# Optimization experiments

Measured on AMD Instinct MI355X. Metric: run time of the kernel, lower is better.

## Reference

```python
import jax, jax.numpy as jnp
import numpy as np
from jax import lax

T_STEPS = 16
TAU = 2.0
ALPHA = 4.0  # sigmoid surrogate sharpness
BN_EPS = 1e-5


def conv1d(x, w, b, stride, pad):
    # x: [N,C,L], w: [O,I,K]
    y = lax.conv_general_dilated(x, w, (stride,), [(pad, pad)],
                                 dimension_numbers=('NCH', 'OIH', 'NCH'))
    return y + b[None, :, None]


def maxpool1d(x):  # kernel 3, stride 2, pad 1 (pad value -inf via init)
    return lax.reduce_window(x, -jnp.inf, lax.max, (1, 1, 3), (1, 1, 2),
                             [(0, 0), (0, 0), (1, 1)])


def spike(x):  # heaviside forward (surrogate only matters for bwd)
    return (x >= 0).astype(x.dtype)


def lif(x_seq):
    # multi-step LIF: v += (x - v)/tau (v_reset=0), spike at v>=1, hard reset, detach_reset
    def step(v, x):
        v = v + (x - v) / TAU
        s = spike(v - 1.0)
        v = v * (1.0 - lax.stop_gradient(s))
        return v, s
    _, s_seq = lax.scan(step, jnp.zeros_like(x_seq[0]), x_seq)
    return s_seq


def seq_apply(f, xs):
    # apply stateless layer over [T,B,...] by folding T into batch
    T, B = xs.shape[0], xs.shape[1]
    y = f(xs.reshape((T * B,) + xs.shape[2:]))
    return y.reshape((T, B) + y.shape[1:])


def setup_inputs() -> dict:
    key = jax.random.key(0)
    ks = jax.random.split(key, 12)
    B, L = 256, 4097
    inp = {
        'x': jax.random.normal(ks[0], (B, L), jnp.float32),
        'conv0_w': jax.random.normal(ks[1], (16, 1, 7), jnp.float32) * 0.2,
        'conv0_b': jax.random.normal(ks[2], (16,), jnp.float32) * 0.1,
        'bn_g': jnp.ones((16,), jnp.float32),
        'bn_b': jnp.zeros((16,), jnp.float32),
        'bn_m': jax.random.normal(ks[3], (16,), jnp.float32) * 0.1,
        'bn_v': jnp.ones((16,), jnp.float32),
        'conv1_w': jax.random.normal(ks[4], (32, 16, 5), jnp.float32) * 0.1,
        'conv1_b': jax.random.normal(ks[5], (32,), jnp.float32) * 0.1,
        'conv2_w': jax.random.normal(ks[6], (64, 32, 3), jnp.float32) * 0.1,
        'conv2_b': jax.random.normal(ks[7], (64,), jnp.float32) * 0.1,
        'fc1_w': jax.random.normal(ks[8], (32, 64), jnp.float32) * 0.12,
        'fc1_b': jax.random.normal(ks[9], (32,), jnp.float32) * 0.1,
        'fc2_w': jax.random.normal(ks[10], (5, 32), jnp.float32) * 0.17,
        'fc2_b': jax.random.normal(ks[11], (5,), jnp.float32) * 0.1,
    }
    return inp


def reference(x, conv0_w, conv0_b, bn_g, bn_b, bn_m, bn_v,
              conv1_w, conv1_b, conv2_w, conv2_b,
              fc1_w, fc1_b, fc2_w, fc2_b):
    # ---- static encoder ----
    h = x[:, None, :]                                  # [B,1,4097]
    h = conv1d(h, conv0_w, conv0_b, 2, 3)              # [B,16,2049]
    h = (h - bn_m[None, :, None]) * lax.rsqrt(bn_v + BN_EPS)[None, :, None] \
        * bn_g[None, :, None] + bn_b[None, :, None]
    h = jax.nn.relu(h)
    h = maxpool1d(h)                                   # [B,16,1025]
    # ---- repeat over T timesteps ----
    hs = jnp.broadcast_to(h[None], (T_STEPS,) + h.shape)  # [T,B,16,1025]
    # ---- spiking trunk ----
    hs = seq_apply(lambda a: conv1d(a, conv1_w, conv1_b, 2, 2), hs)  # [T,B,32,513]
    hs = lif(hs)
    hs = seq_apply(maxpool1d, hs)                      # [T,B,32,257]
    hs = seq_apply(lambda a: conv1d(a, conv2_w, conv2_b, 2, 1), hs)  # [T,B,64,129]
    hs = lif(hs)
    # dropout: identity (inference); adaptive avg pool to 1 + flatten
    hs = hs.mean(axis=-1)                              # [T,B,64]
    # ---- classifier ----
    hs = jnp.einsum('tbd,od->tbo', hs, fc1_w) + fc1_b  # [T,B,32]
    hs = lif(hs)
    hs = jnp.einsum('tbd,od->tbo', hs, fc2_w) + fc2_b  # [T,B,5]
    return hs.mean(axis=0)                             # [B,5]
```

## Files before the change

### kernel.cpp

```cpp
#include <hip/hip_runtime.h>
#include <math.h>


#define NB 256
#define LX 4097
#define LQ 2049
#define LP 1025
#define LJ1 513
#define LP1 257
#define LJ2 129

#define M1S 520
#define S2R 132
#define JT 64
#define NJT 9
#define HSW 132
#define XSN 544

typedef float f32x4 __attribute__((ext_vector_type(4)));

__global__ __launch_bounds__(256) void kS_setup(const float* __restrict__ w1,
                                                const float* __restrict__ w2,
                                                float* __restrict__ w1t,
                                                float* __restrict__ w2t2) {
  int tid = threadIdx.x;
  for (int i = tid; i < 2560; i += 256) {
    int c = i & 31, r = i >> 5;
    w1t[i] = w1[c * 80 + r];
  }
  for (int idx = tid; idx < 64 * 32 * 3; idx += 256) {
    int k = idx % 3; int r = idx / 3; int cc = r % 32; int oc = r / 32;
    w2t2[((size_t)cc * 64 + oc) * 4 + k] = w2[idx];
  }
}

__global__ __launch_bounds__(256) void kF_front(const float* __restrict__ x,
                                                const float* __restrict__ w0,
                                                const float* __restrict__ b0,
                                                const float* __restrict__ bng,
                                                const float* __restrict__ bnb,
                                                const float* __restrict__ bnm,
                                                const float* __restrict__ bnv,
                                                const float* __restrict__ w1t_g,
                                                const float* __restrict__ b1,
                                                unsigned short* __restrict__ m1) {
  __shared__ __align__(16) float xs[XSN];
  __shared__ __align__(16) float hs[16 * HSW];
  __shared__ float w0s[112];
  __shared__ float cpar[64];
  __shared__ float rs_l[16];
  int bid = blockIdx.x;
  int b = bid / NJT, jt = bid % NJT;
  int J0 = jt * JT;
  int Pstart = 2 * J0 - 2;
  int tid = threadIdx.x;

  if (tid < 16) rs_l[tid] = (float)(1.0 / sqrt((double)bnv[tid] + 1e-5));
  {
    const float* xb = x + (size_t)b * LX;
    int xoff = 4 * Pstart - 5;
    for (int i = tid; i < XSN; i += 256) {
      int gi = xoff + i;
      xs[i] = (gi >= 0 && gi < LX) ? xb[gi] : 0.f;
    }
    if (tid < 112) w0s[tid] = w0[tid];
    if (tid >= 128 && tid < 192) {
      int i = tid - 128;
      int c = i >> 2, e = i & 3;
      float v = (e == 0) ? bnm[c] : (e == 1) ? bng[c] : (e == 2) ? bnb[c] : b0[c];
      cpar[i] = v;
    }
  }
  __syncthreads();

  {
    int c2 = tid >> 4, g2 = tid & 15;
    float m = cpar[4 * c2], g = cpar[4 * c2 + 1], bb = cpar[4 * c2 + 2],
          bc = cpar[4 * c2 + 3];
    float rs = rs_l[c2];
    float wv[7];
#pragma unroll
    for (int k = 0; k < 7; ++k) wv[k] = w0s[c2 * 7 + k];
    int dp0 = g2 * 9;
    const f32x4* xv = (const f32x4*)xs;
    f32x4 q0 = xv[dp0], q1 = xv[dp0 + 1], q2 = xv[dp0 + 2];
#pragma unroll
    for (int i = 0; i < 9; ++i) {
      int dp = dp0 + i;
      if (dp >= 132) break;
      int p = Pstart + dp;
      float hm = 0.f;
      if (p >= 0 && p < LP) {
        float win[12] = {q0.x, q0.y, q0.z, q0.w, q1.x, q1.y, q1.z, q1.w,
                         q2.x, q2.y, q2.z, q2.w};
        float best = -INFINITY;
#pragma unroll
        for (int dq = -1; dq <= 1; ++dq) {
          int q = 2 * p + dq;
          if (q < 0 || q >= LQ) continue;
          float s = 0.f;
          int base = 2 * dq + 2;
#pragma unroll
          for (int k = 0; k < 7; ++k) s = fmaf(win[base + k], wv[k], s);
          float y = s + bc;
          y = (y - m) * rs * g + bb;
          y = fmaxf(y, 0.f);
          best = fmaxf(best, y);
        }
        hm = best;
      }
      hs[c2 * HSW + dp] = hm;
      q0 = q1; q1 = q2; q2 = xv[dp + 3];
    }
  }
  __syncthreads();

  {
    int c = tid & 31, jg = tid >> 5;
    int jbase = J0 + jg * 8;
    if (jbase <= 512) {
      float acc[8];
#pragma unroll
      for (int i = 0; i < 8; ++i) acc[i] = 0.f;

#pragma unroll 1
      for (int ic = 0; ic < 16; ++ic) {
        float win[20];
        const f32x4* row = (const f32x4*)(hs + ic * HSW + 16 * jg);
#pragma unroll
        for (int i = 0; i < 5; ++i) {
          f32x4 v = row[i];
          win[4 * i] = v.x; win[4 * i + 1] = v.y;
          win[4 * i + 2] = v.z; win[4 * i + 3] = v.w;
        }
        float wv[5];
#pragma unroll
        for (int k = 0; k < 5; ++k) wv[k] = w1t_g[(ic * 5 + k) * 32 + c];
#pragma unroll
        for (int j = 0; j < 8; ++j) {
#pragma unroll
          for (int k = 0; k < 5; ++k) acc[j] = fmaf(win[2 * j + k], wv[k], acc[j]);
        }
      }

      float bc = b1[c];
      unsigned mskv[8];
#pragma unroll
      for (int j = 0; j < 8; ++j) {
        float xin = acc[j] + bc;
        float v = 0.f; unsigned mm = 0;
#pragma unroll
        for (int t = 0; t < 16; ++t) {
          v = v + (xin - v) * 0.5f;
          if (v >= 1.f) { mm |= (1u << t); v = 0.f; }
        }
        mskv[j] = mm;
      }
      size_t rowo = ((size_t)b * 32 + c) * M1S + jbase;
      if (jbase + 7 < LJ1) {
        uint4 u0;
        u0.x = mskv[0] | (mskv[1] << 16);
        u0.y = mskv[2] | (mskv[3] << 16);
        u0.z = mskv[4] | (mskv[5] << 16);
        u0.w = mskv[6] | (mskv[7] << 16);
        *(uint4*)(m1 + rowo) = u0;
      } else {
        for (int j = 0; j < 8; ++j)
          if (jbase + j < LJ1) m1[rowo + j] = (unsigned short)mskv[j];
      }
    }
  }
}

__global__ __launch_bounds__(256) void kD_conv2_lif(const unsigned short* __restrict__ m1,
                                                    const float* __restrict__ w2t2,
                                                    const float* __restrict__ b2,
                                                    unsigned short* __restrict__ s2) {
  __shared__ __align__(16) float F[288 * 20];
  __shared__ unsigned mval[288];
  int bid = blockIdx.x;
  int b = bid / 33, jt = bid % 33;
  int j0 = jt * 4;
  int tid = threadIdx.x;
  int w = tid >> 6;
  int lane = tid & 63;

  const unsigned short* m1b = m1 + (size_t)b * 32 * M1S;

  for (int it = tid; it < 288; it += 256) {
    int c = it / 9, idx = it - c * 9;
    int p = 2 * j0 - 1 + idx;
    unsigned m = 0;
    if (p >= 0 && p < LP1) {
      const unsigned short* mr = m1b + (size_t)c * M1S;
      int q0 = 2 * p - 1;
      if (q0 >= 0) m |= mr[q0];
      m |= mr[q0 + 1];
      if (q0 + 2 <= 512) m |= mr[q0 + 2];
    }
    mval[it] = m;
    f32x4* Fr = (f32x4*)(F + it * 20);
    f32x4 f0, f1, f2, f3;
    f0.x = (float)(m & 1u);         f0.y = (float)((m >> 1) & 1u);
    f0.z = (float)((m >> 2) & 1u);  f0.w = (float)((m >> 3) & 1u);
    f1.x = (float)((m >> 4) & 1u);  f1.y = (float)((m >> 5) & 1u);
    f1.z = (float)((m >> 6) & 1u);  f1.w = (float)((m >> 7) & 1u);
    f2.x = (float)((m >> 8) & 1u);  f2.y = (float)((m >> 9) & 1u);
    f2.z = (float)((m >> 10) & 1u); f2.w = (float)((m >> 11) & 1u);
    f3.x = (float)((m >> 12) & 1u); f3.y = (float)((m >> 13) & 1u);
    f3.z = (float)((m >> 14) & 1u); f3.w = (float)((m >> 15) & 1u);
    Fr[0] = f0; Fr[1] = f1; Fr[2] = f2; Fr[3] = f3;
  }
  __syncthreads();

  unsigned bits;
  {
    bool nz = false;
    if (lane < 32) {
      int base9 = lane * 9 + 2 * w;
      nz = (mval[base9] | mval[base9 + 1] | mval[base9 + 2]) != 0u;
    }
    bits = (unsigned)__ballot(nz);
  }

  float acc[16];
#pragma unroll
  for (int t = 0; t < 16; ++t) acc[t] = 0.f;

  const f32x4* wbase = (const f32x4*)w2t2 + lane;
  while (bits) {
    int c = __builtin_ctz(bits);
    bits &= bits - 1;
    int base9 = c * 9 + 2 * w;
    unsigned mv0 = mval[base9];
    unsigned mv1 = mval[base9 + 1];
    unsigned mv2 = mval[base9 + 2];
    f32x4 wq = wbase[c * 64];
    const float* Fb = F + base9 * 20;
    if (mv0) {
      const f32x4* Fp = (const f32x4*)Fb;
      f32x4 fv[4];
      fv[0] = Fp[0]; fv[1] = Fp[1]; fv[2] = Fp[2]; fv[3] = Fp[3];
#pragma unroll
      for (int t = 0; t < 16; ++t) acc[t] = fmaf(wq.x, fv[t >> 2][t & 3], acc[t]);
    }
    if (mv1) {
      const f32x4* Fp = (const f32x4*)(Fb + 20);
      f32x4 fv[4];
      fv[0] = Fp[0]; fv[1] = Fp[1]; fv[2] = Fp[2]; fv[3] = Fp[3];
#pragma unroll
      for (int t = 0; t < 16; ++t) acc[t] = fmaf(wq.y, fv[t >> 2][t & 3], acc[t]);
    }
    if (mv2) {
      const f32x4* Fp = (const f32x4*)(Fb + 40);
      f32x4 fv[4];
      fv[0] = Fp[0]; fv[1] = Fp[1]; fv[2] = Fp[2]; fv[3] = Fp[3];
#pragma unroll
      for (int t = 0; t < 16; ++t) acc[t] = fmaf(wq.z, fv[t >> 2][t & 3], acc[t]);
    }
  }

  int j = j0 + w;
  if (j < LJ2) {
    float bc = b2[lane];
    float v = 0.f; unsigned mm = 0;
#pragma unroll
    for (int t = 0; t < 16; ++t) {
      float xin = acc[t] + bc;
      v = v + (xin - v) * 0.5f;
      if (v >= 1.f) { mm |= (1u << t); v = 0.f; }
    }
    s2[((size_t)b * S2R + j) * 64 + lane] = (unsigned short)mm;
  }
}

__global__ __launch_bounds__(256) void kE_head(const unsigned short* __restrict__ s2,
                                               const float* __restrict__ fc1w,
                                               const float* __restrict__ fc1b,
                                               const float* __restrict__ fc2w,
                                               const float* __restrict__ fc2b,
                                               float* __restrict__ out) {
  __shared__ unsigned cntL[4][16][64];
  __shared__ float meanL[16][64];
  __shared__ unsigned s3m[32];
  int b = blockIdx.x;
  int tid = threadIdx.x;
  int w = tid >> 6, lane = tid & 63;

  int j0 = (w == 0) ? 0 : 33 + 32 * (w - 1);
  int jc = (w == 0) ? 33 : 32;
  const unsigned short* base = s2 + (size_t)b * S2R * 64 + lane;
  unsigned cnt[16];
#pragma unroll
  for (int t = 0; t < 16; ++t) cnt[t] = 0;
  for (int u = 0; u < jc; ++u) {
    unsigned m = base[(size_t)(j0 + u) * 64];
#pragma unroll
    for (int t = 0; t < 16; ++t) cnt[t] += (m >> t) & 1u;
  }
#pragma unroll
  for (int t = 0; t < 16; ++t) cntL[w][t][lane] = cnt[t];
  __syncthreads();

#pragma unroll
  for (int i = 0; i < 4; ++i) {
    int idx = tid + 256 * i;
    int t = idx >> 6, oc = idx & 63;
    unsigned s = cntL[0][t][oc] + cntL[1][t][oc] + cntL[2][t][oc] + cntL[3][t][oc];
    meanL[t][oc] = (float)s / 129.f;
  }
  __syncthreads();

  if (tid < 32) {
    int o = tid;
    const float* wrow = fc1w + o * 64;
    float bb = fc1b[o];
    float v = 0.f;
    unsigned msk = 0;
    for (int t = 0; t < 16; ++t) {
      float s = 0.f;
      for (int d = 0; d < 64; ++d) s = fmaf(meanL[t][d], wrow[d], s);
      float xin = s + bb;
      v = v + (xin - v) * 0.5f;
      if (v >= 1.f) { msk |= (1u << t); v = 0.f; }
    }
    s3m[o] = msk;
  }
  __syncthreads();

  if (tid < 5) {
    int q = tid;
    const float* wrow = fc2w + q * 32;
    float bb = fc2b[q];
    float accs = 0.f;
    for (int t = 0; t < 16; ++t) {
      float s = 0.f;
      for (int o = 0; o < 32; ++o) s += (((s3m[o] >> t) & 1u) ? wrow[o] : 0.f);
      accs += (s + bb);
    }
    out[b * 5 + q] = accs / 16.f;
  }
}

extern "C" void kernel_launch(void* const* d_in, const int* in_sizes, int n_in,
                              void* d_out, int out_size, void* d_ws, size_t ws_size,
                              hipStream_t stream) {
  const float* x   = (const float*)d_in[0];
  const float* w0  = (const float*)d_in[1];
  const float* b0  = (const float*)d_in[2];
  const float* bng = (const float*)d_in[3];
  const float* bnb = (const float*)d_in[4];
  const float* bnm = (const float*)d_in[5];
  const float* bnv = (const float*)d_in[6];
  const float* w1  = (const float*)d_in[7];
  const float* b1  = (const float*)d_in[8];
  const float* w2  = (const float*)d_in[9];
  const float* b2  = (const float*)d_in[10];
  const float* f1w = (const float*)d_in[11];
  const float* f1b = (const float*)d_in[12];
  const float* f2w = (const float*)d_in[13];
  const float* f2b = (const float*)d_in[14];
  float* out = (float*)d_out;

  char* ws = (char*)d_ws;
  size_t sz_m1 = (size_t)NB * 32 * M1S * 2;
  size_t sz_s2 = (size_t)NB * S2R * 64 * 2;
  size_t off_s2 = sz_m1;
  size_t off_w2 = off_s2 + sz_s2;
  size_t off_w1 = off_w2 + 32768;
  if (ws_size < off_w1 + 10240) return;

  unsigned short* m1 = (unsigned short*)ws;
  unsigned short* s2 = (unsigned short*)(ws + off_s2);
  float* w2t2 = (float*)(ws + off_w2);
  float* w1t  = (float*)(ws + off_w1);

  kS_setup<<<1, 256, 0, stream>>>(w1, w2, w1t, w2t2);
  kF_front<<<NB * NJT, 256, 0, stream>>>(x, w0, b0, bng, bnb, bnm, bnv, w1t, b1, m1);
  kD_conv2_lif<<<NB * 33, 256, 0, stream>>>(m1, w2t2, b2, s2);
  kE_head<<<NB, 256, 0, stream>>>(s2, f1w, f1b, f2w, f2b, out);
}
```

Measured before the change: 108.8 us.

## Fold weight setup kernel into front kernel and stage conv1 weights in LDS

Drops the single-block setup kernel. Each front-kernel block now loads and transposes conv1 weights into shared memory itself, and the first 16 blocks write the transposed conv2 weights for the next kernel. This removes one launch and its serialization, and turns the global weight reads in the conv1 inner loop into shared-memory reads. The cost is extra per-block weight loading and about 10KB more LDS per block, which may reduce occupancy. The conv2 kernel also replaces per-iteration LDS mask reads with three ballots.

```diff
diff --git a/kernel.cpp b/kernel.cpp
--- a/kernel.cpp
+++ b/kernel.cpp
@@ -19,21 +19,6 @@
 
 typedef float f32x4 __attribute__((ext_vector_type(4)));
 
-__global__ __launch_bounds__(256) void kS_setup(const float* __restrict__ w1,
-                                                const float* __restrict__ w2,
-                                                float* __restrict__ w1t,
-                                                float* __restrict__ w2t2) {
-  int tid = threadIdx.x;
-  for (int i = tid; i < 2560; i += 256) {
-    int c = i & 31, r = i >> 5;
-    w1t[i] = w1[c * 80 + r];
-  }
-  for (int idx = tid; idx < 64 * 32 * 3; idx += 256) {
-    int k = idx % 3; int r = idx / 3; int cc = r % 32; int oc = r / 32;
-    w2t2[((size_t)cc * 64 + oc) * 4 + k] = w2[idx];
-  }
-}
-
 __global__ __launch_bounds__(256) void kF_front(const float* __restrict__ x,
                                                 const float* __restrict__ w0,
                                                 const float* __restrict__ b0,
@@ -41,11 +26,14 @@
                                                 const float* __restrict__ bnb,
                                                 const float* __restrict__ bnm,
                                                 const float* __restrict__ bnv,
-                                                const float* __restrict__ w1t_g,
+                                                const float* __restrict__ w1,
                                                 const float* __restrict__ b1,
-                                                unsigned short* __restrict__ m1) {
+                                                unsigned short* __restrict__ m1,
+                                                const float* __restrict__ w2,
+                                                float* __restrict__ w2t2) {
   __shared__ __align__(16) float xs[XSN];
   __shared__ __align__(16) float hs[16 * HSW];
+  __shared__ __align__(16) float wl[2560];
   __shared__ float w0s[112];
   __shared__ float cpar[64];
   __shared__ float rs_l[16];
@@ -62,6 +50,9 @@
     for (int i = tid; i < XSN; i += 256) {
       int gi = xoff + i;
       xs[i] = (gi >= 0 && gi < LX) ? xb[gi] : 0.f;
+    }
+    for (int i = tid; i < 2560; i += 256) {
+      wl[i] = w1[(i & 31) * 80 + (i >> 5)];
     }
     if (tid < 112) w0s[tid] = w0[tid];
     if (tid >= 128 && tid < 192) {
@@ -135,7 +126,7 @@
         }
         float wv[5];
 #pragma unroll
-        for (int k = 0; k < 5; ++k) wv[k] = w1t_g[(ic * 5 + k) * 32 + c];
+        for (int k = 0; k < 5; ++k) wv[k] = wl[(ic * 5 + k) * 32 + c];
 #pragma unroll
         for (int j = 0; j < 8; ++j) {
 #pragma unroll
@@ -170,6 +161,13 @@
       }
     }
   }
+
+  if (bid < 16) {
+    for (int idx = bid * 256 + tid; idx < 64 * 32 * 3; idx += 4096) {
+      int k = idx % 3; int r = idx / 3; int cc = r % 32; int oc = r / 32;
+      w2t2[((size_t)cc * 64 + oc) * 4 + k] = w2[idx];
+    }
+  }
 }
 
 __global__ __launch_bounds__(256) void kD_conv2_lif(const unsigned short* __restrict__ m1,
@@ -213,15 +211,17 @@
   }
   __syncthreads();
 
-  unsigned bits;
-  {
-    bool nz = false;
-    if (lane < 32) {
-      int base9 = lane * 9 + 2 * w;
-      nz = (mval[base9] | mval[base9 + 1] | mval[base9 + 2]) != 0u;
-    }
-    bits = (unsigned)__ballot(nz);
-  }
+  bool nz0 = false, nz1 = false, nz2 = false;
+  if (lane < 32) {
+    int mb = lane * 9 + 2 * w;
+    nz0 = mval[mb] != 0u;
+    nz1 = mval[mb + 1] != 0u;
+    nz2 = mval[mb + 2] != 0u;
+  }
+  unsigned bz0 = (unsigned)__ballot(nz0);
+  unsigned bz1 = (unsigned)__ballot(nz1);
+  unsigned bz2 = (unsigned)__ballot(nz2);
+  unsigned bits = bz0 | bz1 | bz2;
 
   float acc[16];
 #pragma unroll
@@ -232,26 +232,23 @@
     int c = __builtin_ctz(bits);
     bits &= bits - 1;
     int base9 = c * 9 + 2 * w;
-    unsigned mv0 = mval[base9];
-    unsigned mv1 = mval[base9 + 1];
-    unsigned mv2 = mval[base9 + 2];
     f32x4 wq = wbase[c * 64];
     const float* Fb = F + base9 * 20;
-    if (mv0) {
+    if ((bz0 >> c) & 1u) {
       const f32x4* Fp = (const f32x4*)Fb;
       f32x4 fv[4];
       fv[0] = Fp[0]; fv[1] = Fp[1]; fv[2] = Fp[2]; fv[3] = Fp[3];
 #pragma unroll
       for (int t = 0; t < 16; ++t) acc[t] = fmaf(wq.x, fv[t >> 2][t & 3], acc[t]);
     }
-    if (mv1) {
+    if ((bz1 >> c) & 1u) {
       const f32x4* Fp = (const f32x4*)(Fb + 20);
       f32x4 fv[4];
       fv[0] = Fp[0]; fv[1] = Fp[1]; fv[2] = Fp[2]; fv[3] = Fp[3];
 #pragma unroll
       for (int t = 0; t < 16; ++t) acc[t] = fmaf(wq.y, fv[t >> 2][t & 3], acc[t]);
     }
-    if (mv2) {
+    if ((bz2 >> c) & 1u) {
       const f32x4* Fp = (const f32x4*)(Fb + 40);
       f32x4 fv[4];
       fv[0] = Fp[0]; fv[1] = Fp[1]; fv[2] = Fp[2]; fv[3] = Fp[3];
@@ -367,16 +364,13 @@
   size_t sz_s2 = (size_t)NB * S2R * 64 * 2;
   size_t off_s2 = sz_m1;
   size_t off_w2 = off_s2 + sz_s2;
-  size_t off_w1 = off_w2 + 32768;
-  if (ws_size < off_w1 + 10240) return;
+  if (ws_size < off_w2 + 32768) return;
 
   unsigned short* m1 = (unsigned short*)ws;
   unsigned short* s2 = (unsigned short*)(ws + off_s2);
   float* w2t2 = (float*)(ws + off_w2);
-  float* w1t  = (float*)(ws + off_w1);
-
-  kS_setup<<<1, 256, 0, stream>>>(w1, w2, w1t, w2t2);
-  kF_front<<<NB * NJT, 256, 0, stream>>>(x, w0, b0, bng, bnb, bnm, bnv, w1t, b1, m1);
+
+  kF_front<<<NB * NJT, 256, 0, stream>>>(x, w0, b0, bng, bnb, bnm, bnv, w1, b1, m1, w2, w2t2);
   kD_conv2_lif<<<NB * 33, 256, 0, stream>>>(m1, w2t2, b2, s2);
   kE_head<<<NB, 256, 0, stream>>>(s2, f1w, f1b, f2w, f2b, out);
 }
```

New measurement: 106.1 us, median of 2. 2.5% less time.
